# Kernel optimization log

Hardware: AMD Instinct MI355X
Metric: run time of the kernel (lower is better)

Reference implementation:

```python
import jax, jax.numpy as jnp
import numpy as np
from jax import lax

B, C, H, W = 4, 64, 128, 128
O, KH, KW = 64, 3, 3
STRIDE, PAD, DIL = 1, 1, 1
KK = KH * KW


def conv2d(x, w, b, stride, pad, dil):
    y = lax.conv_general_dilated(
        x, w, window_strides=(stride, stride),
        padding=[(pad, pad), (pad, pad)], rhs_dilation=(dil, dil),
        dimension_numbers=('NCHW', 'OIHW', 'NCHW'))
    if b is not None:
        y = y + b[None, :, None, None]
    return y


def deform_conv2d(x, offset, mask, weight, stride, pad, dil):
    # x: [B,C,H,W]; offset: [B,2*KK,Ho,Wo] as (dy,dx) pairs per tap (torchvision order);
    # mask: [B,KK,Ho,Wo]; weight: [O,C,KH,KW]
    Bx, Cx, Hx, Wx = x.shape
    Ou, _, kh, kw = weight.shape
    kk = kh * kw
    Ho, Wo = offset.shape[2], offset.shape[3]
    off = offset.reshape(Bx, kk, 2, Ho, Wo)
    off_y, off_x = off[:, :, 0], off[:, :, 1]
    ky = (jnp.arange(kk) // kw).astype(x.dtype) * dil  # [KK]
    kx = (jnp.arange(kk) % kw).astype(x.dtype) * dil
    base_y = (jnp.arange(Ho).astype(x.dtype) * stride - pad)  # [Ho]
    base_x = (jnp.arange(Wo).astype(x.dtype) * stride - pad)
    py = off_y + ky[None, :, None, None] + base_y[None, None, :, None]  # [B,KK,Ho,Wo]
    px = off_x + kx[None, :, None, None] + base_x[None, None, None, :]
    y0 = jnp.floor(py).astype(jnp.int32)
    x0 = jnp.floor(px).astype(jnp.int32)
    y1, x1 = y0 + 1, x0 + 1
    wy1 = py - y0.astype(x.dtype)
    wx1 = px - x0.astype(x.dtype)
    wy0, wx0 = 1.0 - wy1, 1.0 - wx1
    x_flat = x.reshape(Bx, Cx, Hx * Wx)

    def gather(yi, xi):
        valid = ((yi >= 0) & (yi < Hx) & (xi >= 0) & (xi < Wx)).astype(x.dtype)
        idx = jnp.clip(yi, 0, Hx - 1) * Wx + jnp.clip(xi, 0, Wx - 1)  # [B,KK,Ho,Wo]
        v = jax.vmap(lambda xf, i: xf[:, i])(x_flat, idx.reshape(Bx, -1))  # [B,C,KK*Ho*Wo]
        return v.reshape(Bx, Cx, kk, Ho, Wo) * valid[:, None]

    val = (gather(y0, x0) * (wy0 * wx0)[:, None]
           + gather(y0, x1) * (wy0 * wx1)[:, None]
           + gather(y1, x0) * (wy1 * wx0)[:, None]
           + gather(y1, x1) * (wy1 * wx1)[:, None])  # [B,C,KK,Ho,Wo]
    val = val * mask[:, None]
    return jnp.einsum('bckhw,ock->bohw', val, weight.reshape(Ou, Cx, kk))


def setup_inputs() -> dict:
    key = jax.random.key(0)
    ks = jax.random.split(key, 8)
    x = jax.random.normal(ks[0], (B, C, H, W), jnp.float32)
    guide = jax.random.normal(ks[1], (B, C, H, W), jnp.float32)
    # NOTE: module inits offset/modulator convs to zero; we use small random
    # weights so the deformable sampling path is actually exercised.
    w_off = jax.random.normal(ks[2], (2 * KK, 2 * C, KH, KW), jnp.float32) * 0.01
    b_off = jax.random.normal(ks[3], (2 * KK,), jnp.float32) * 0.1
    w_mod = jax.random.normal(ks[4], (KK, 2 * C, KH, KW), jnp.float32) * 0.01
    b_mod = jax.random.normal(ks[5], (KK,), jnp.float32) * 0.1
    fan_in = C * KH * KW
    w_reg = jax.random.normal(ks[6], (O, C, KH, KW), jnp.float32) / np.sqrt(fan_in)
    return {"x": x, "guide": guide, "w_off": w_off, "b_off": b_off,
            "w_mod": w_mod, "b_mod": b_mod, "w_reg": w_reg}


def reference(x, guide, w_off, b_off, w_mod, b_mod, w_reg):
    fea = jnp.concatenate([x, guide], axis=1)  # [B,2C,H,W]
    offset = conv2d(fea, w_off, b_off, STRIDE, PAD, DIL)       # [B,2KK,Ho,Wo]
    modulator = 2.0 * jax.nn.sigmoid(conv2d(fea, w_mod, b_mod, STRIDE, PAD, DIL))
    return deform_conv2d(x, offset, modulator, w_reg, STRIDE, PAD, DIL)
```

## Files before the change

kernel.cpp:

```cpp
#include <hip/hip_runtime.h>
#include <math.h>

#define Bn   4
#define Cc   64
#define Hh   128
#define Ww   128
#define Oo   64
#define HW   16384
#define NPAR 27

#define WB2_OFF 0
#define WB_OFF  18432

typedef __attribute__((ext_vector_type(8))) short bf16x8;
typedef __attribute__((ext_vector_type(4))) short s16x4;
typedef __attribute__((ext_vector_type(4))) float f32x4;
typedef __attribute__((ext_vector_type(2), aligned(4))) float f32x2u;

__device__ __forceinline__ short f2bf(float f) {
    unsigned u = __builtin_bit_cast(unsigned, f);
    u += 0x7FFFu + ((u >> 16) & 1u);
    return (short)(u >> 16);
}

__global__ void prep_weights(const float* __restrict__ w_off,
                             const float* __restrict__ w_mod,
                             const float* __restrict__ w_reg,
                             float* __restrict__ ws) {
    int i = blockIdx.x * 256 + threadIdx.x;
    short* at2 = (short*)(ws + WB2_OFF);
    short* atd = (short*)(ws + WB_OFF);
    if (i < 36864) {
        int j = i & 7, l = (i >> 3) & 63, mt = (i >> 9) & 1, cc = (i >> 10) & 3, t = i >> 12;
        int lm = l & 15, quad = l >> 4;
        int row = mt * 16 + lm;
        int c = cc * 32 + quad * 8 + j;
        float v = 0.f;
        if (row < 18)      v = w_off[row * 1152 + c * 9 + t];
        else if (row < 27) v = w_mod[(row - 18) * 1152 + c * 9 + t];
        at2[i] = f2bf(v);
    } else if (i < 73728) {
        int e = i - 36864;
        int j = e & 7, l = (e >> 3) & 63, mt = (e >> 9) & 3, h = (e >> 11) & 1, t = e >> 12;
        int lm = l & 15, quad = l >> 4;
        int o = mt * 16 + lm;
        int c = h * 32 + quad * 8 + j;
        atd[e] = f2bf(w_reg[o * 576 + c * 9 + t]);
    }
}

#define CPSTR 136
#define DPSTR 36

struct TapP {
    float wa0, wb0, wa1, wb1;
    int ia, ib, gx0, gx1;
    bool in;
};

__device__ __forceinline__ TapP tap_params_v(float py, float px, float m,
                                             int rb, int cb) {
    float fy = floorf(py), fx = floorf(px);
    int y0 = (int)fy, x0 = (int)fx;
    int y1 = y0 + 1;
    float wy1 = py - fy, wx1 = px - fx;
    float wy0 = 1.f - wy1, wx0 = 1.f - wx1;
    bool vy0 = (unsigned)y0 < 128u, vy1 = (unsigned)y1 < 128u;
    bool vx0 = (unsigned)x0 < 128u, vx1 = (unsigned)(x0 + 1) < 128u;
    int cy0 = min(max(y0, 0), 127), cy1 = min(max(y1, 0), 127);
    int bx2 = min(max(x0, 0), 126);
    bool sel_lo = (x0 < 0), sel_hi = (x0 > 126);
    float w00 = (vy0 && vx0) ? wy0 * wx0 * m : 0.f;
    float w01 = (vy0 && vx1) ? wy0 * wx1 * m : 0.f;
    float w10 = (vy1 && vx0) ? wy1 * wx0 * m : 0.f;
    float w11 = (vy1 && vx1) ? wy1 * wx1 * m : 0.f;
    TapP r;
    r.wa0 = sel_lo ? w01 : (sel_hi ? 0.f : w00);
    r.wb0 = sel_hi ? w00 : (sel_lo ? 0.f : w01);
    r.wa1 = sel_lo ? w11 : (sel_hi ? 0.f : w10);
    r.wb1 = sel_hi ? w10 : (sel_lo ? 0.f : w11);
    int ty0 = cy0 - rb, ty1 = cy1 - rb, tx = bx2 - cb;
    r.ia = ty0 * 24 + tx;
    r.ib = ty1 * 24 + tx;
    r.gx0 = (cy0 << 7) + bx2;
    r.gx1 = (cy1 << 7) + bx2;
    r.in = ((unsigned)ty0 <= 9u) && ((unsigned)ty1 <= 9u) && ((unsigned)tx <= 22u);
    return r;
}

__device__ __forceinline__ void lds_corners(const TapP& P, const float* Xw,
                                            int quad, f32x4* c) {
    int ia = min(max(P.ia, 0), 238);
    int ib = min(max(P.ib, 0), 238);
    const float* pa = Xw + ia * DPSTR + quad * 8;
    const float* pb = Xw + ib * DPSTR + quad * 8;
    c[0] = *(const f32x4*)(pa);
    c[1] = *(const f32x4*)(pa + DPSTR);
    c[2] = *(const f32x4*)(pb);
    c[3] = *(const f32x4*)(pb + DPSTR);
    c[4] = *(const f32x4*)(pa + 4);
    c[5] = *(const f32x4*)(pa + DPSTR + 4);
    c[6] = *(const f32x4*)(pb + 4);
    c[7] = *(const f32x4*)(pb + DPSTR + 4);
}

__device__ __forceinline__ void fix_corners(const TapP& P, const float* __restrict__ xb,
                                            int h, int quad, f32x4* c) {
    if (__builtin_expect(!P.in, 0)) {
#pragma unroll
        for (int hf = 0; hf < 2; hf++)
#pragma unroll
            for (int j = 0; j < 4; j++) {
                int cch = h * 32 + quad * 8 + hf * 4 + j;
                const float* xc = xb + ((size_t)cch << 14);
                f32x2u q0 = *(const f32x2u*)(xc + P.gx0);
                f32x2u q1 = *(const f32x2u*)(xc + P.gx1);
                c[hf * 4 + 0][j] = q0.x;
                c[hf * 4 + 1][j] = q0.y;
                c[hf * 4 + 2][j] = q1.x;
                c[hf * 4 + 3][j] = q1.y;
            }
    }
}

__global__ __attribute__((amdgpu_waves_per_eu(4, 4))) __launch_bounds__(256)
void fused_dcn(const float* __restrict__ x, const float* __restrict__ g,
               const float* __restrict__ ws_,
               const float* __restrict__ b_off, const float* __restrict__ b_mod,
               float* __restrict__ out) {
    __shared__ __align__(16) char Ubuf[144 * CPSTR * 2];
    short* Wd = (short*)Ubuf;
    float* Xw = (float*)Ubuf;

    const int tid = threadIdx.x;
    const int l = tid & 63, lm = l & 15, quad = l >> 4;
    const int w = __builtin_amdgcn_readfirstlane(tid >> 6);
    const int b = blockIdx.z;
    const int ho0 = blockIdx.y * 4, wo0 = blockIdx.x * 16;

    const short* at2 = (const short*)(ws_ + WB2_OFF);
    const short* atd = (const short*)(ws_ + WB_OFF);
    const float* xb = x + ((size_t)(b * Cc) << 14);
    const float* gb = g + ((size_t)(b * Cc) << 14);

    {
        const int row_base = ho0 - 1;
        const int col_base = wo0 - 4;
        for (int s = tid; s < 1152; s += 256) {
            int pq = s >> 5, cq = s & 31;
            int r = pq / 6, c4 = (pq - r * 6) * 4;
            int row = row_base + r, col = col_base + c4;
            bool ok = ((unsigned)row < 128u) && ((unsigned)col < 128u);
            f32x4 v0, v1, v2, v3;
            {
                int ch = cq * 4;
                const float* p0 = (ch < Cc) ? (xb + ((size_t)ch << 14)) : (gb + ((size_t)(ch - Cc) << 14));
                const float* p1 = (ch + 1 < Cc) ? (xb + ((size_t)(ch + 1) << 14)) : (gb + ((size_t)(ch + 1 - Cc) << 14));
                const float* p2 = (ch + 2 < Cc) ? (xb + ((size_t)(ch + 2) << 14)) : (gb + ((size_t)(ch + 2 - Cc) << 14));
                const float* p3 = (ch + 3 < Cc) ? (xb + ((size_t)(ch + 3) << 14)) : (gb + ((size_t)(ch + 3 - Cc) << 14));
                f32x4 zz = {0.f, 0.f, 0.f, 0.f};
                size_t off = ((size_t)(row << 7) + col);
                v0 = ok ? *(const f32x4*)(p0 + off) : zz;
                v1 = ok ? *(const f32x4*)(p1 + off) : zz;
                v2 = ok ? *(const f32x4*)(p2 + off) : zz;
                v3 = ok ? *(const f32x4*)(p3 + off) : zz;
            }
#pragma unroll
            for (int p = 0; p < 4; p++) {
                s16x4 o4 = { f2bf(v0[p]), f2bf(v1[p]), f2bf(v2[p]), f2bf(v3[p]) };
                *(s16x4*)&Wd[(r * 24 + c4 + p) * CPSTR + cq * 4] = o4;
            }
        }
    }
    __syncthreads();

    f32x4 acc0 = {0.f, 0.f, 0.f, 0.f}, acc1 = {0.f, 0.f, 0.f, 0.f};
#pragma unroll
    for (int t = 0; t < 9; t++) {
        int dy = t / 3, dx = t - dy * 3;
        int pos = (w + dy) * 24 + (lm + dx + 3);
#pragma unroll
        for (int cc = 0; cc < 4; cc++) {
            bf16x8 bfr = *(const bf16x8*)&Wd[pos * CPSTR + cc * 32 + quad * 8];
            bf16x8 a0 = *(const bf16x8*)(at2 + t * 4096 + cc * 1024 + l * 8);
            bf16x8 a1 = *(const bf16x8*)(at2 + t * 4096 + cc * 1024 + 512 + l * 8);
            acc0 = __builtin_amdgcn_mfma_f32_16x16x32_bf16(a0, bfr, acc0, 0, 0, 0);
            acc1 = __builtin_amdgcn_mfma_f32_16x16x32_bf16(a1, bfr, acc1, 0, 0, 0);
        }
    }

    const int ho = ho0 + w, wo = wo0 + lm;
    float tv[8];
#pragma unroll
    for (int mt = 0; mt < 2; mt++) {
        f32x4 a = mt ? acc1 : acc0;
#pragma unroll
        for (int reg = 0; reg < 4; reg++) {
            int j = mt * 16 + quad * 4 + reg;
            float v = a[reg];
            float r = 0.f;
            if (j < 18) {
                int k = j >> 1;
                float vb = v + b_off[j];
                r = (j & 1) ? (vb + (float)(k - (k / 3) * 3 + wo - 1))
                            : (vb + (float)(k / 3 + ho - 1));
            } else if (j < 27) {
                int k = j - 18;
                r = 2.f / (1.f + __expf(-(v + b_mod[k])));
            }
            tv[mt * 4 + reg] = r;
        }
    }

    float pr[27];
#pragma unroll
    for (int c = 0; c < 27; c++) {
        int j = (c < 9) ? (2 * c) : ((c < 18) ? (2 * (c - 9) + 1) : c);
        int srcLane = (((j >> 2) & 3) << 4) | lm;
        pr[c] = __shfl(tv[(j >> 4) * 4 + (j & 3)], srcLane);
    }

    __syncthreads();

    const int rb = min(max(ho0 - 3, 0), 128 - 10);
    const int cb = min(max(wo0 - 4, 0), 128 - 24);

    auto STAGE = [&](int h) {
        for (int s = tid; s < 480; s += 256) {
            int pq = s >> 3, cq = s & 7;
            int r = pq / 6, c4 = (pq - r * 6) * 4;
            size_t off = (size_t)((rb + r) << 7) + cb + c4;
            f32x4 v0 = *(const f32x4*)(xb + ((size_t)(h * 32 + cq * 4 + 0) << 14) + off);
            f32x4 v1 = *(const f32x4*)(xb + ((size_t)(h * 32 + cq * 4 + 1) << 14) + off);
            f32x4 v2 = *(const f32x4*)(xb + ((size_t)(h * 32 + cq * 4 + 2) << 14) + off);
            f32x4 v3 = *(const f32x4*)(xb + ((size_t)(h * 32 + cq * 4 + 3) << 14) + off);
#pragma unroll
            for (int p = 0; p < 4; p++) {
                f32x4 o4 = { v0[p], v1[p], v2[p], v3[p] };
                *(f32x4*)&Xw[(r * 24 + c4 + p) * DPSTR + cq * 4] = o4;
            }
        }
    };

    STAGE(0);
    __syncthreads();

    f32x4 acc[4];
#pragma unroll
    for (int mt = 0; mt < 4; mt++) acc[mt] = (f32x4){0.f, 0.f, 0.f, 0.f};

    auto T_LOOP = [&](int h) {
#pragma unroll
        for (int t = 0; t < 9; t++) {
            TapP P = tap_params_v(pr[t], pr[9 + t], pr[18 + t], rb, cb);
            f32x4 c[8];
            lds_corners(P, Xw, quad, c);
            fix_corners(P, xb, h, quad, c);
            union { short s8[8]; bf16x8 v; } u;
#pragma unroll
            for (int hf = 0; hf < 2; hf++)
#pragma unroll
                for (int j = 0; j < 4; j++)
                    u.s8[hf * 4 + j] = f2bf(P.wa0 * c[hf * 4 + 0][j] + P.wb0 * c[hf * 4 + 1][j] +
                                            P.wa1 * c[hf * 4 + 2][j] + P.wb1 * c[hf * 4 + 3][j]);
#pragma unroll
            for (int mt = 0; mt < 4; mt++) {
                bf16x8 a = *(const bf16x8*)(atd + t * 4096 + h * 2048 + mt * 512 + l * 8);
                acc[mt] = __builtin_amdgcn_mfma_f32_16x16x32_bf16(a, u.v, acc[mt], 0, 0, 0);
            }
        }
    };

    T_LOOP(0);
    __syncthreads();
    STAGE(1);
    __syncthreads();
    T_LOOP(1);

#pragma unroll
    for (int mt = 0; mt < 4; mt++) {
        float* op = out + ((size_t)(b * Oo + mt * 16 + quad * 4) << 14) + (ho << 7) + wo;
#pragma unroll
        for (int reg = 0; reg < 4; reg++)
            op[(size_t)reg << 14] = acc[mt][reg];
    }
}

extern "C" void kernel_launch(void* const* d_in, const int* in_sizes, int n_in,
                              void* d_out, int out_size, void* d_ws, size_t ws_size,
                              hipStream_t stream) {
    const float* x     = (const float*)d_in[0];
    const float* guide = (const float*)d_in[1];
    const float* w_off = (const float*)d_in[2];
    const float* b_off = (const float*)d_in[3];
    const float* w_mod = (const float*)d_in[4];
    const float* b_mod = (const float*)d_in[5];
    const float* w_reg = (const float*)d_in[6];
    float* out = (float*)d_out;
    float* ws  = (float*)d_ws;

    hipLaunchKernelGGL(prep_weights, dim3((73728 + 255) / 256), dim3(256),
                       0, stream, w_off, w_mod, w_reg, ws);
    hipLaunchKernelGGL(fused_dcn, dim3(Ww / 16, Hh / 4, Bn), dim3(256),
                       0, stream, x, guide, ws, b_off, b_mod, out);
}
```

Baseline: 153.9 us.

## Stage per-pixel sampling params in LDS and shrink deformable tile window

The 27 per-pixel offset/mask values are no longer shuffled into 27 registers per lane. They are written once to shared memory and reread per tap. The staged x window shrinks from 10 to 8 rows, and corner loads are split into halves to cut live registers. The wave-occupancy attribute becomes a launch_bounds minimum of 4 blocks. This trades register pressure for extra LDS reads and more fallback global gathers when offsets fall outside the smaller window.

Measured after the change: 140.7 us. 1.09x faster.

```diff
diff --git a/kernel.cpp b/kernel.cpp
--- a/kernel.cpp
+++ b/kernel.cpp
@@ -51,6 +51,9 @@
 
 #define CPSTR 136
 #define DPSTR 36
+#define DROWS 8
+#define PAR_STR 29
+#define XW_OFF (64 * PAR_STR)
 
 struct TapP {
     float wa0, wb0, wa1, wb1;
@@ -84,53 +87,21 @@
     r.ib = ty1 * 24 + tx;
     r.gx0 = (cy0 << 7) + bx2;
     r.gx1 = (cy1 << 7) + bx2;
-    r.in = ((unsigned)ty0 <= 9u) && ((unsigned)ty1 <= 9u) && ((unsigned)tx <= 22u);
+    r.in = ((unsigned)ty0 <= (unsigned)(DROWS - 1)) &&
+           ((unsigned)ty1 <= (unsigned)(DROWS - 1)) &&
+           ((unsigned)tx <= 22u);
     return r;
 }
 
-__device__ __forceinline__ void lds_corners(const TapP& P, const float* Xw,
-                                            int quad, f32x4* c) {
-    int ia = min(max(P.ia, 0), 238);
-    int ib = min(max(P.ib, 0), 238);
-    const float* pa = Xw + ia * DPSTR + quad * 8;
-    const float* pb = Xw + ib * DPSTR + quad * 8;
-    c[0] = *(const f32x4*)(pa);
-    c[1] = *(const f32x4*)(pa + DPSTR);
-    c[2] = *(const f32x4*)(pb);
-    c[3] = *(const f32x4*)(pb + DPSTR);
-    c[4] = *(const f32x4*)(pa + 4);
-    c[5] = *(const f32x4*)(pa + DPSTR + 4);
-    c[6] = *(const f32x4*)(pb + 4);
-    c[7] = *(const f32x4*)(pb + DPSTR + 4);
-}
-
-__device__ __forceinline__ void fix_corners(const TapP& P, const float* __restrict__ xb,
-                                            int h, int quad, f32x4* c) {
-    if (__builtin_expect(!P.in, 0)) {
-#pragma unroll
-        for (int hf = 0; hf < 2; hf++)
-#pragma unroll
-            for (int j = 0; j < 4; j++) {
-                int cch = h * 32 + quad * 8 + hf * 4 + j;
-                const float* xc = xb + ((size_t)cch << 14);
-                f32x2u q0 = *(const f32x2u*)(xc + P.gx0);
-                f32x2u q1 = *(const f32x2u*)(xc + P.gx1);
-                c[hf * 4 + 0][j] = q0.x;
-                c[hf * 4 + 1][j] = q0.y;
-                c[hf * 4 + 2][j] = q1.x;
-                c[hf * 4 + 3][j] = q1.y;
-            }
-    }
-}
-
-__global__ __attribute__((amdgpu_waves_per_eu(4, 4))) __launch_bounds__(256)
+__global__ __launch_bounds__(256, 4)
 void fused_dcn(const float* __restrict__ x, const float* __restrict__ g,
                const float* __restrict__ ws_,
                const float* __restrict__ b_off, const float* __restrict__ b_mod,
                float* __restrict__ out) {
     __shared__ __align__(16) char Ubuf[144 * CPSTR * 2];
-    short* Wd = (short*)Ubuf;
-    float* Xw = (float*)Ubuf;
+    short* Wd   = (short*)Ubuf;
+    float* parL = (float*)Ubuf;
+    float* Xw   = (float*)Ubuf + XW_OFF;
 
     const int tid = threadIdx.x;
     const int l = tid & 63, lm = l & 15, quad = l >> 4;
@@ -190,7 +161,8 @@
     }
 
     const int ho = ho0 + w, wo = wo0 + lm;
-    float tv[8];
+    const int pxi = w * 16 + lm;
+    float tr[8];
 #pragma unroll
     for (int mt = 0; mt < 2; mt++) {
         f32x4 a = mt ? acc1 : acc0;
@@ -208,25 +180,28 @@
                 int k = j - 18;
                 r = 2.f / (1.f + __expf(-(v + b_mod[k])));
             }
-            tv[mt * 4 + reg] = r;
-        }
-    }
-
-    float pr[27];
-#pragma unroll
-    for (int c = 0; c < 27; c++) {
-        int j = (c < 9) ? (2 * c) : ((c < 18) ? (2 * (c - 9) + 1) : c);
-        int srcLane = (((j >> 2) & 3) << 4) | lm;
-        pr[c] = __shfl(tv[(j >> 4) * 4 + (j & 3)], srcLane);
-    }
-
-    __syncthreads();
-
-    const int rb = min(max(ho0 - 3, 0), 128 - 10);
+            tr[mt * 4 + reg] = r;
+        }
+    }
+
+    __syncthreads();
+
+#pragma unroll
+    for (int mt = 0; mt < 2; mt++)
+#pragma unroll
+        for (int reg = 0; reg < 4; reg++) {
+            int j = mt * 16 + quad * 4 + reg;
+            if (j < 27) {
+                int c = (j < 18) ? ((j & 1) ? (9 + (j >> 1)) : (j >> 1)) : j;
+                parL[pxi * PAR_STR + c] = tr[mt * 4 + reg];
+            }
+        }
+
+    const int rb = min(max(ho0 - 2, 0), 128 - DROWS);
     const int cb = min(max(wo0 - 4, 0), 128 - 24);
 
     auto STAGE = [&](int h) {
-        for (int s = tid; s < 480; s += 256) {
+        for (int s = tid; s < DROWS * 6 * 8; s += 256) {
             int pq = s >> 3, cq = s & 7;
             int r = pq / 6, c4 = (pq - r * 6) * 4;
             size_t off = (size_t)((rb + r) << 7) + cb + c4;
@@ -252,17 +227,36 @@
     auto T_LOOP = [&](int h) {
 #pragma unroll
         for (int t = 0; t < 9; t++) {
-            TapP P = tap_params_v(pr[t], pr[9 + t], pr[18 + t], rb, cb);
-            f32x4 c[8];
-            lds_corners(P, Xw, quad, c);
-            fix_corners(P, xb, h, quad, c);
+            float py = parL[pxi * PAR_STR + t];
+            float px = parL[pxi * PAR_STR + 9 + t];
+            float m  = parL[pxi * PAR_STR + 18 + t];
+            TapP P = tap_params_v(py, px, m, rb, cb);
+            int ia = min(max(P.ia, 0), DROWS * 24 - 2);
+            int ib = min(max(P.ib, 0), DROWS * 24 - 2);
             union { short s8[8]; bf16x8 v; } u;
 #pragma unroll
-            for (int hf = 0; hf < 2; hf++)
+            for (int hf = 0; hf < 2; hf++) {
+                const float* pa = Xw + ia * DPSTR + quad * 8 + hf * 4;
+                const float* pb = Xw + ib * DPSTR + quad * 8 + hf * 4;
+                f32x4 c0 = *(const f32x4*)(pa);
+                f32x4 c1 = *(const f32x4*)(pa + DPSTR);
+                f32x4 c2 = *(const f32x4*)(pb);
+                f32x4 c3 = *(const f32x4*)(pb + DPSTR);
+                if (__builtin_expect(!P.in, 0)) {
+#pragma unroll
+                    for (int j = 0; j < 4; j++) {
+                        int cch = h * 32 + quad * 8 + hf * 4 + j;
+                        const float* xc = xb + ((size_t)cch << 14);
+                        f32x2u q0 = *(const f32x2u*)(xc + P.gx0);
+                        f32x2u q1 = *(const f32x2u*)(xc + P.gx1);
+                        c0[j] = q0.x; c1[j] = q0.y; c2[j] = q1.x; c3[j] = q1.y;
+                    }
+                }
 #pragma unroll
                 for (int j = 0; j < 4; j++)
-                    u.s8[hf * 4 + j] = f2bf(P.wa0 * c[hf * 4 + 0][j] + P.wb0 * c[hf * 4 + 1][j] +
-                                            P.wa1 * c[hf * 4 + 2][j] + P.wb1 * c[hf * 4 + 3][j]);
+                    u.s8[hf * 4 + j] = f2bf(P.wa0 * c0[j] + P.wb0 * c1[j] +
+                                            P.wa1 * c2[j] + P.wb1 * c3[j]);
+            }
 #pragma unroll
             for (int mt = 0; mt < 4; mt++) {
                 bf16x8 a = *(const bf16x8*)(atd + t * 4096 + h * 2048 + mt * 512 + l * 8);
```
